# Kernel optimization log

Hardware: AMD Instinct MI355X
Metric: run time of the kernel (lower is better)

The kernel has to match this reference:

```python
import jax, jax.numpy as jnp
import numpy as np

D_MODEL = 1024
EPS = 1e-5  # torch LayerNorm default


def layernorm(x, gamma, beta):
    mu = jnp.mean(x, axis=-1, keepdims=True)
    var = jnp.mean(jnp.square(x - mu), axis=-1, keepdims=True)
    return (x - mu) * jax.lax.rsqrt(var + EPS) * gamma + beta


def setup_inputs() -> dict:
    key = jax.random.key(0)
    ks = jax.random.split(key, 9)
    B, S, D = 4, 2048, D_MODEL
    s = 1.0 / np.sqrt(D)  # ~ nn.Linear default init scale
    return {
        "x": jax.random.normal(ks[0], (B, S, D), dtype=jnp.float32),
        "wq_w": jax.random.uniform(ks[1], (D, D), jnp.float32, -s, s),
        "wq_b": jax.random.uniform(ks[2], (D,), jnp.float32, -s, s),
        "wk_w": jax.random.uniform(ks[3], (D, D), jnp.float32, -s, s),
        "wk_b": jax.random.uniform(ks[4], (D,), jnp.float32, -s, s),
        "wv_w": jax.random.uniform(ks[5], (D, D), jnp.float32, -s, s),
        "wv_b": jax.random.uniform(ks[6], (D,), jnp.float32, -s, s),
        "lin_w": jax.random.uniform(ks[7], (D, D), jnp.float32, -s, s),
        "lin_b": jax.random.uniform(ks[8], (D,), jnp.float32, -s, s),
        "g1": jnp.ones((D,), jnp.float32),
        "b1": jnp.zeros((D,), jnp.float32),
        "g2": jnp.ones((D,), jnp.float32),
        "b2": jnp.zeros((D,), jnp.float32),
    }


def reference(x, wq_w, wq_b, wk_w, wk_b, wv_w, wv_b, lin_w, lin_b, g1, b1, g2, b2):
    # single-head attention over full d_model (num_heads unused in original forward)
    q = jnp.einsum("bsd,ed->bse", x, wq_w) + wq_b
    k = jnp.einsum("bsd,ed->bse", x, wk_w) + wk_b
    v = jnp.einsum("bsd,ed->bse", x, wv_w) + wv_b
    scale = 1.0 / jnp.sqrt(jnp.float32(x.shape[-1]))
    scores = jax.nn.softmax(jnp.einsum("bqd,bkd->bqk", q, k) * scale, axis=2)
    attention = jnp.einsum("bqk,bkd->bqd", scores, v)
    # faithful to original: tril applied to the [S, D] attention OUTPUT per batch
    attention = jnp.tril(attention)
    x = layernorm(x + attention, g1, b1)
    linear_output = jnp.einsum("bsd,ed->bse", x, lin_w) + lin_b
    x = layernorm(x + linear_output, g2, b2)
    return x
```

## Files before the change

kernel.cpp:

```cpp
#include <hip/hip_runtime.h>
#include <hip/hip_bf16.h>

#define SEQ 2048
#define DM 1024
#define NB 4

typedef short bf16x8 __attribute__((ext_vector_type(8)));
typedef float f32x4 __attribute__((ext_vector_type(4)));
typedef float f32x4v __attribute__((ext_vector_type(4)));
typedef unsigned short u16x4 __attribute__((ext_vector_type(4)));
typedef unsigned short u16x8 __attribute__((ext_vector_type(8)));

__device__ __forceinline__ float bf2f(unsigned short u) {
  union { unsigned int i; float f; } w; w.i = ((unsigned int)u) << 16; return w.f;
}
__device__ __forceinline__ unsigned short f2bf(float f) {
  union { __hip_bfloat16 h; unsigned short u; } w; w.h = __float2bfloat16(f); return w.u;
}
__device__ __forceinline__ void load_lds16(const void* g, void* l) {
  __builtin_amdgcn_global_load_lds((const __attribute__((address_space(1))) void*)g,
                                   (__attribute__((address_space(3))) void*)l, 16, 0, 0);
}

__global__ __launch_bounds__(256) void cvt_kernel(const float* __restrict__ in,
                                                  unsigned short* __restrict__ out, int n4) {
  int idx = blockIdx.x * 256 + threadIdx.x;
  int stride = gridDim.x * 256;
  for (int i = idx; i < n4; i += stride) {
    f32x4v x = ((const f32x4v*)in)[i];
    u16x4 o;
    o[0] = f2bf(x[0]); o[1] = f2bf(x[1]); o[2] = f2bf(x[2]); o[3] = f2bf(x[3]);
    ((u16x4*)out)[i] = o;
  }
}

__global__ __launch_bounds__(256, 2) void gemm_bt(
    const unsigned short* __restrict__ A, int lda, long sA,
    const unsigned short* __restrict__ B, int ldb, long sB,
    void* __restrict__ Cv, int ldc, long sC,
    int K, const float* __restrict__ bias, float scale, int outf32)
{
  __shared__ unsigned short As[128 * 64];
  __shared__ unsigned short Bs[128 * 64];
  const int tid = threadIdx.x;
  const int lane = tid & 63;
  const int wave = tid >> 6;
  const int wm = wave >> 1, wn = wave & 1;
  const int m0 = blockIdx.x * 128, n0 = blockIdx.y * 128;
  const unsigned short* Ab = A + (size_t)sA * blockIdx.z;
  const unsigned short* Bb = B + (size_t)sB * blockIdx.z;

  f32x4 acc[4][4];
#pragma unroll
  for (int i = 0; i < 4; ++i)
#pragma unroll
    for (int j = 0; j < 4; ++j)
      acc[i][j] = (f32x4){0.f, 0.f, 0.f, 0.f};

  const int nk = K >> 6;
  for (int kt = 0; kt < nk; ++kt) {
    __syncthreads();
    const int kb = kt << 6;
#pragma unroll
    for (int it = 0; it < 4; ++it) {
      int c = it * 256 + tid;
      int row = c >> 3;
      int lslot = (c & 7) ^ (row & 7);
      int ldsoff = (it * 256 + wave * 64) * 8;
      load_lds16(Ab + (size_t)(m0 + row) * lda + kb + lslot * 8, &As[ldsoff]);
      load_lds16(Bb + (size_t)(n0 + row) * ldb + kb + lslot * 8, &Bs[ldsoff]);
    }
    __syncthreads();
#pragma unroll
    for (int h = 0; h < 2; ++h) {
      bf16x8 af[4], bfr[4];
#pragma unroll
      for (int i = 0; i < 4; ++i) {
        int row = wm * 64 + i * 16 + (lane & 15);
        int pslot = (h * 4 + (lane >> 4)) ^ (row & 7);
        af[i] = *(const bf16x8*)&As[row * 64 + pslot * 8];
      }
#pragma unroll
      for (int j = 0; j < 4; ++j) {
        int row = wn * 64 + j * 16 + (lane & 15);
        int pslot = (h * 4 + (lane >> 4)) ^ (row & 7);
        bfr[j] = *(const bf16x8*)&Bs[row * 64 + pslot * 8];
      }
#pragma unroll
      for (int i = 0; i < 4; ++i)
#pragma unroll
        for (int j = 0; j < 4; ++j)
          acc[i][j] = __builtin_amdgcn_mfma_f32_16x16x32_bf16(af[i], bfr[j], acc[i][j], 0, 0, 0);
    }
  }

  const int rsub = (lane >> 4) * 4;
  const int cbase = n0 + wn * 64 + (lane & 15);
  if (outf32) {
    float* C = (float*)Cv + (size_t)sC * blockIdx.z;
#pragma unroll
    for (int i = 0; i < 4; ++i) {
      int rbase = m0 + wm * 64 + i * 16 + rsub;
#pragma unroll
      for (int j = 0; j < 4; ++j)
#pragma unroll
        for (int r = 0; r < 4; ++r)
          C[(size_t)(rbase + r) * ldc + cbase + j * 16] = acc[i][j][r] * scale;
    }
  } else {
    unsigned short* C = (unsigned short*)Cv + (size_t)sC * blockIdx.z;
    float bv[4] = {0.f, 0.f, 0.f, 0.f};
    if (bias) {
#pragma unroll
      for (int j = 0; j < 4; ++j) bv[j] = bias[cbase + j * 16];
    }
#pragma unroll
    for (int i = 0; i < 4; ++i) {
      int rbase = m0 + wm * 64 + i * 16 + rsub;
#pragma unroll
      for (int j = 0; j < 4; ++j)
#pragma unroll
        for (int r = 0; r < 4; ++r)
          C[(size_t)(rbase + r) * ldc + cbase + j * 16] = f2bf(acc[i][j][r] + bv[j]);
    }
  }
}

__global__ __launch_bounds__(256) void transpose_kernel(const unsigned short* __restrict__ v,
                                                        int lda, long sV,
                                                        unsigned short* __restrict__ vt) {
  __shared__ unsigned short t[64][65];
  int b = blockIdx.z;
  int s0 = blockIdx.x * 64;
  int d0 = blockIdx.y * 64;
  int tid = threadIdx.x;
  int rr = tid >> 3;
  int c8 = (tid & 7) * 8;
  const unsigned short* vb = v + (size_t)sV * b;
#pragma unroll
  for (int it = 0; it < 2; ++it) {
    int row = rr + it * 32;
    u16x8 val = *(const u16x8*)&vb[(size_t)(s0 + row) * lda + d0 + c8];
#pragma unroll
    for (int j = 0; j < 8; ++j) t[row][c8 + j] = val[j];
  }
  __syncthreads();
#pragma unroll
  for (int it = 0; it < 2; ++it) {
    int drow = rr + it * 32;
    u16x8 o;
#pragma unroll
    for (int j = 0; j < 8; ++j) o[j] = t[c8 + j][drow];
    *(u16x8*)&vt[((size_t)b * DM + d0 + drow) * SEQ + s0 + c8] = o;
  }
}

__global__ __launch_bounds__(256) void softmax_kernel(const float* __restrict__ Sc,
                                                      unsigned short* __restrict__ P) {
  int row = blockIdx.x;
  int tid = threadIdx.x;
  const float* sr = Sc + (size_t)row * SEQ;
  float v[8];
  f32x4v a = ((const f32x4v*)sr)[tid * 2];
  f32x4v b = ((const f32x4v*)sr)[tid * 2 + 1];
  v[0]=a[0]; v[1]=a[1]; v[2]=a[2]; v[3]=a[3];
  v[4]=b[0]; v[5]=b[1]; v[6]=b[2]; v[7]=b[3];
  float m = v[0];
#pragma unroll
  for (int j = 1; j < 8; ++j) m = fmaxf(m, v[j]);
#pragma unroll
  for (int off = 32; off; off >>= 1) m = fmaxf(m, __shfl_xor(m, off));
  __shared__ float red[8];
  int wv = tid >> 6;
  if ((tid & 63) == 0) red[wv] = m;
  __syncthreads();
  m = fmaxf(fmaxf(red[0], red[1]), fmaxf(red[2], red[3]));
  float s = 0.f;
#pragma unroll
  for (int j = 0; j < 8; ++j) { v[j] = __expf(v[j] - m); s += v[j]; }
#pragma unroll
  for (int off = 32; off; off >>= 1) s += __shfl_xor(s, off);
  if ((tid & 63) == 0) red[4 + wv] = s;
  __syncthreads();
  s = red[4] + red[5] + red[6] + red[7];
  float inv = 1.f / s;
  u16x8 o;
#pragma unroll
  for (int j = 0; j < 8; ++j) o[j] = f2bf(v[j] * inv);
  *(u16x8*)&P[(size_t)row * SEQ + tid * 8] = o;
}

__global__ __launch_bounds__(256) void ln_kernel(
    const float* __restrict__ xf, const unsigned short* __restrict__ xb,
    const unsigned short* __restrict__ res, int masked,
    const float* __restrict__ g, const float* __restrict__ be,
    float* __restrict__ outf, unsigned short* __restrict__ outb)
{
  int row = blockIdx.x;
  int s = row & (SEQ - 1);
  int tid = threadIdx.x;
  int d0 = tid * 4;
  float v[4];
  if (xf) {
    f32x4v t = ((const f32x4v*)(xf + (size_t)row * DM))[tid];
    v[0]=t[0]; v[1]=t[1]; v[2]=t[2]; v[3]=t[3];
  } else {
    u16x4 t = ((const u16x4*)(xb + (size_t)row * DM))[tid];
    v[0]=bf2f(t[0]); v[1]=bf2f(t[1]); v[2]=bf2f(t[2]); v[3]=bf2f(t[3]);
  }
  u16x4 rv = ((const u16x4*)(res + (size_t)row * DM))[tid];
#pragma unroll
  for (int j = 0; j < 4; ++j) {
    float r = bf2f(rv[j]);
    if (masked && (d0 + j) > s) r = 0.f;
    v[j] += r;
  }
  float s1 = v[0] + v[1] + v[2] + v[3];
  float s2 = v[0]*v[0] + v[1]*v[1] + v[2]*v[2] + v[3]*v[3];
#pragma unroll
  for (int off = 32; off; off >>= 1) { s1 += __shfl_xor(s1, off); s2 += __shfl_xor(s2, off); }
  __shared__ float red[8];
  int wv = tid >> 6;
  if ((tid & 63) == 0) { red[wv] = s1; red[4 + wv] = s2; }
  __syncthreads();
  s1 = red[0] + red[1] + red[2] + red[3];
  s2 = red[4] + red[5] + red[6] + red[7];
  float mean = s1 * (1.f / DM);
  float var = s2 * (1.f / DM) - mean * mean;
  float rstd = rsqrtf(var + 1e-5f);
  f32x4v gv = ((const f32x4v*)g)[tid];
  f32x4v bv = ((const f32x4v*)be)[tid];
  if (outf) {
    f32x4v o;
#pragma unroll
    for (int j = 0; j < 4; ++j) o[j] = (v[j] - mean) * rstd * gv[j] + bv[j];
    ((f32x4v*)(outf + (size_t)row * DM))[tid] = o;
  } else {
    u16x4 o;
#pragma unroll
    for (int j = 0; j < 4; ++j) o[j] = f2bf((v[j] - mean) * rstd * gv[j] + bv[j]);
    ((u16x4*)(outb + (size_t)row * DM))[tid] = o;
  }
}

extern "C" void kernel_launch(void* const* d_in, const int* in_sizes, int n_in,
                              void* d_out, int out_size, void* d_ws, size_t ws_size,
                              hipStream_t stream) {
  (void)in_sizes; (void)n_in; (void)out_size; (void)ws_size;
  const float* x     = (const float*)d_in[0];
  const float* wq_w  = (const float*)d_in[1];
  const float* wq_b  = (const float*)d_in[2];
  const float* wk_w  = (const float*)d_in[3];
  const float* wk_b  = (const float*)d_in[4];
  const float* wv_w  = (const float*)d_in[5];
  const float* wv_b  = (const float*)d_in[6];
  const float* lin_w = (const float*)d_in[7];
  const float* lin_b = (const float*)d_in[8];
  const float* g1    = (const float*)d_in[9];
  const float* b1    = (const float*)d_in[10];
  const float* g2    = (const float*)d_in[11];
  const float* b2    = (const float*)d_in[12];

  const size_t MB = 1ull << 20;
  char* ws = (char*)d_ws;
  float*          sc   = (float*)(ws);
  unsigned short* attn = (unsigned short*)(ws);
  unsigned short* lin  = (unsigned short*)(ws + 16*MB);
  unsigned short* x1   = (unsigned short*)(ws + 32*MB);
  unsigned short* wqkvb= (unsigned short*)(ws + 48*MB);
  unsigned short* xb   = (unsigned short*)(ws + 54*MB);
  unsigned short* P    = (unsigned short*)(ws + 64*MB);
  unsigned short* qkv  = (unsigned short*)(ws + 96*MB);
  unsigned short* vt   = (unsigned short*)(ws + 144*MB);
  unsigned short* lwb  = (unsigned short*)(ws + 160*MB);
  float*          bqkv = (float*)(ws + 162*MB);

  const size_t SD = (size_t)NB * SEQ * DM;

  cvt_kernel<<<2048, 256, 0, stream>>>(x, xb, (int)(SD / 4));
  cvt_kernel<<<1024, 256, 0, stream>>>(wq_w, wqkvb, DM * DM / 4);
  cvt_kernel<<<1024, 256, 0, stream>>>(wk_w, wqkvb + DM * DM, DM * DM / 4);
  cvt_kernel<<<1024, 256, 0, stream>>>(wv_w, wqkvb + 2 * DM * DM, DM * DM / 4);
  cvt_kernel<<<1024, 256, 0, stream>>>(lin_w, lwb, DM * DM / 4);
  hipMemcpyAsync(bqkv,        wq_b, DM * sizeof(float), hipMemcpyDeviceToDevice, stream);
  hipMemcpyAsync(bqkv + DM,   wk_b, DM * sizeof(float), hipMemcpyDeviceToDevice, stream);
  hipMemcpyAsync(bqkv + 2*DM, wv_b, DM * sizeof(float), hipMemcpyDeviceToDevice, stream);

  gemm_bt<<<dim3(64, 24, 1), 256, 0, stream>>>(xb, DM, 0, wqkvb, DM, 0, qkv, 3 * DM, 0,
                                               DM, bqkv, 1.f, 0);
  transpose_kernel<<<dim3(SEQ / 64, DM / 64, NB), 256, 0, stream>>>(
      qkv + 2 * DM, 3 * DM, (long)SEQ * 3 * DM, vt);

  const float scale = 0.03125f;
  gemm_bt<<<dim3(16, 16, NB), 256, 0, stream>>>(
      qkv, 3 * DM, (long)SEQ * 3 * DM,
      qkv + DM, 3 * DM, (long)SEQ * 3 * DM,
      sc, SEQ, (long)SEQ * SEQ, DM, nullptr, scale, 1);
  softmax_kernel<<<NB * SEQ, 256, 0, stream>>>(sc, P);
  gemm_bt<<<dim3(16, 8, NB), 256, 0, stream>>>(
      P, SEQ, (long)SEQ * SEQ,
      vt, SEQ, (long)DM * SEQ,
      attn, DM, (long)SEQ * DM, SEQ, nullptr, 1.f, 0);

  ln_kernel<<<NB * SEQ, 256, 0, stream>>>(x, nullptr, attn, 1, g1, b1, nullptr, x1);
  gemm_bt<<<dim3(64, 8, 1), 256, 0, stream>>>(x1, DM, 0, lwb, DM, 0, lin, DM, 0, DM, lin_b, 1.f, 0);
  ln_kernel<<<NB * SEQ, 256, 0, stream>>>(nullptr, x1, lin, 0, g2, b2, (float*)d_out, nullptr);
}
```

Before: 235.7 us.

## Add 256-tile pipelined score GEMM, bf16 in-place scores, skip masked PV tiles

The QK^T scores GEMM moves to a new 256x256-tile, 512-thread kernel that double-buffers LDS loads and raises wave priority around the MFMA blocks. It writes scaled scores as bf16, and softmax then runs in place on that buffer, so the fp32 score matrix and the separate P buffer are no longer needed. The P·V GEMM gains a trilskip flag that exits early on output tiles lying entirely above the diagonal, since tril zeroes those attention outputs anyway. The trade-off is extra rounding of the pre-softmax scores to bf16. Skipped tiles also leave their attn entries unwritten, and this is only safe if the masked layernorm never reads those positions.

```diff
diff --git a/kernel.cpp b/kernel.cpp
--- a/kernel.cpp
+++ b/kernel.cpp
@@ -38,15 +38,16 @@
     const unsigned short* __restrict__ A, int lda, long sA,
     const unsigned short* __restrict__ B, int ldb, long sB,
     void* __restrict__ Cv, int ldc, long sC,
-    int K, const float* __restrict__ bias, float scale, int outf32)
+    int K, const float* __restrict__ bias, float scale, int outf32, int trilskip)
 {
+  const int m0 = blockIdx.x * 128, n0 = blockIdx.y * 128;
+  if (trilskip && n0 > m0 + 127) return;
   __shared__ unsigned short As[128 * 64];
   __shared__ unsigned short Bs[128 * 64];
   const int tid = threadIdx.x;
   const int lane = tid & 63;
   const int wave = tid >> 6;
   const int wm = wave >> 1, wn = wave & 1;
-  const int m0 = blockIdx.x * 128, n0 = blockIdx.y * 128;
   const unsigned short* Ab = A + (size_t)sA * blockIdx.z;
   const unsigned short* Bb = B + (size_t)sB * blockIdx.z;
 
@@ -121,7 +122,138 @@
       for (int j = 0; j < 4; ++j)
 #pragma unroll
         for (int r = 0; r < 4; ++r)
-          C[(size_t)(rbase + r) * ldc + cbase + j * 16] = f2bf(acc[i][j][r] + bv[j]);
+          C[(size_t)(rbase + r) * ldc + cbase + j * 16] = f2bf(acc[i][j][r] * scale + bv[j]);
+    }
+  }
+}
+
+__global__ __launch_bounds__(512, 2) void gemm256(
+    const unsigned short* __restrict__ A, int lda, long sA,
+    const unsigned short* __restrict__ B, int ldb, long sB,
+    void* __restrict__ Cv, int ldc, long sC,
+    int K, const float* __restrict__ bias, float scale, int outf32)
+{
+  __shared__ unsigned short As[2][256 * 64];
+  __shared__ unsigned short Bs[2][256 * 64];
+  const int tid = threadIdx.x;
+  const int lane = tid & 63;
+  const int wave = tid >> 6;
+  const int wm = wave >> 2;
+  const int wn = wave & 3;
+  const int m0 = blockIdx.x * 256, n0 = blockIdx.y * 256;
+  const unsigned short* Ab = A + (size_t)sA * blockIdx.z;
+  const unsigned short* Bb = B + (size_t)sB * blockIdx.z;
+
+  f32x4 acc[8][4];
+#pragma unroll
+  for (int i = 0; i < 8; ++i)
+#pragma unroll
+    for (int j = 0; j < 4; ++j)
+      acc[i][j] = (f32x4){0.f, 0.f, 0.f, 0.f};
+
+  const int nk = K >> 6;
+
+  auto STAGE = [&](int b, int kt) {
+    const int kb = kt << 6;
+#pragma unroll
+    for (int i = 0; i < 4; ++i) {
+      int c = i * 512 + tid;
+      int row = c >> 3;
+      int lslot = (c & 7) ^ (row & 7);
+      load_lds16(Ab + (size_t)(m0 + row) * lda + kb + lslot * 8, &As[b][c * 8]);
+      load_lds16(Bb + (size_t)(n0 + row) * ldb + kb + lslot * 8, &Bs[b][c * 8]);
+    }
+  };
+
+  STAGE(0, 0);
+  if (nk > 1) {
+    STAGE(1, 1);
+    asm volatile("s_waitcnt vmcnt(8)" ::: "memory");
+  } else {
+    asm volatile("s_waitcnt vmcnt(0)" ::: "memory");
+  }
+  __builtin_amdgcn_sched_barrier(0);
+  __builtin_amdgcn_s_barrier();
+  __builtin_amdgcn_sched_barrier(0);
+
+  for (int kt = 0; kt < nk; ++kt) {
+    const int b = kt & 1;
+    const unsigned short* Asb = As[b];
+    const unsigned short* Bsb = Bs[b];
+    bf16x8 bfr[4][2];
+#pragma unroll
+    for (int j = 0; j < 4; ++j) {
+      int row = wn * 64 + j * 16 + (lane & 15);
+#pragma unroll
+      for (int h = 0; h < 2; ++h) {
+        int pslot = (h * 4 + (lane >> 4)) ^ (row & 7);
+        bfr[j][h] = *(const bf16x8*)&Bsb[row * 64 + pslot * 8];
+      }
+    }
+#pragma unroll
+    for (int q = 0; q < 4; ++q) {
+      bf16x8 af[2][2];
+#pragma unroll
+      for (int i = 0; i < 2; ++i) {
+        int row = wm * 128 + (q * 2 + i) * 16 + (lane & 15);
+#pragma unroll
+        for (int h = 0; h < 2; ++h) {
+          int pslot = (h * 4 + (lane >> 4)) ^ (row & 7);
+          af[i][h] = *(const bf16x8*)&Asb[row * 64 + pslot * 8];
+        }
+      }
+      __builtin_amdgcn_s_setprio(1);
+#pragma unroll
+      for (int i = 0; i < 2; ++i)
+#pragma unroll
+        for (int j = 0; j < 4; ++j)
+#pragma unroll
+          for (int h = 0; h < 2; ++h)
+            acc[q * 2 + i][j] =
+                __builtin_amdgcn_mfma_f32_16x16x32_bf16(af[i][h], bfr[j][h], acc[q * 2 + i][j], 0, 0, 0);
+      __builtin_amdgcn_s_setprio(0);
+    }
+    __builtin_amdgcn_sched_barrier(0);
+    __builtin_amdgcn_s_barrier();
+    __builtin_amdgcn_sched_barrier(0);
+    if (kt + 2 < nk) STAGE(b, kt + 2);
+    if (kt + 1 < nk) {
+      if (kt + 2 < nk) asm volatile("s_waitcnt vmcnt(8)" ::: "memory");
+      else             asm volatile("s_waitcnt vmcnt(0)" ::: "memory");
+      __builtin_amdgcn_sched_barrier(0);
+      __builtin_amdgcn_s_barrier();
+      __builtin_amdgcn_sched_barrier(0);
+    }
+  }
+
+  const int rsub = (lane >> 4) * 4;
+  const int cbase = n0 + wn * 64 + (lane & 15);
+  if (outf32) {
+    float* C = (float*)Cv + (size_t)sC * blockIdx.z;
+#pragma unroll
+    for (int i = 0; i < 8; ++i) {
+      int rbase = m0 + wm * 128 + i * 16 + rsub;
+#pragma unroll
+      for (int j = 0; j < 4; ++j)
+#pragma unroll
+        for (int r = 0; r < 4; ++r)
+          C[(size_t)(rbase + r) * ldc + cbase + j * 16] = acc[i][j][r] * scale;
+    }
+  } else {
+    unsigned short* C = (unsigned short*)Cv + (size_t)sC * blockIdx.z;
+    float bv[4] = {0.f, 0.f, 0.f, 0.f};
+    if (bias) {
+#pragma unroll
+      for (int j = 0; j < 4; ++j) bv[j] = bias[cbase + j * 16];
+    }
+#pragma unroll
+    for (int i = 0; i < 8; ++i) {
+      int rbase = m0 + wm * 128 + i * 16 + rsub;
+#pragma unroll
+      for (int j = 0; j < 4; ++j)
+#pragma unroll
+        for (int r = 0; r < 4; ++r)
+          C[(size_t)(rbase + r) * ldc + cbase + j * 16] = f2bf(acc[i][j][r] * scale + bv[j]);
     }
   }
 }
@@ -155,16 +287,14 @@
   }
 }
 
-__global__ __launch_bounds__(256) void softmax_kernel(const float* __restrict__ Sc,
-                                                      unsigned short* __restrict__ P) {
+__global__ __launch_bounds__(256) void softmax_kernel(unsigned short* __restrict__ Sc) {
   int row = blockIdx.x;
   int tid = threadIdx.x;
-  const float* sr = Sc + (size_t)row * SEQ;
+  unsigned short* sr = Sc + (size_t)row * SEQ;
+  u16x8 raw = *(const u16x8*)&sr[tid * 8];
   float v[8];
-  f32x4v a = ((const f32x4v*)sr)[tid * 2];
-  f32x4v b = ((const f32x4v*)sr)[tid * 2 + 1];
-  v[0]=a[0]; v[1]=a[1]; v[2]=a[2]; v[3]=a[3];
-  v[4]=b[0]; v[5]=b[1]; v[6]=b[2]; v[7]=b[3];
+#pragma unroll
+  for (int j = 0; j < 8; ++j) v[j] = bf2f(raw[j]);
   float m = v[0];
 #pragma unroll
   for (int j = 1; j < 8; ++j) m = fmaxf(m, v[j]);
@@ -187,7 +317,7 @@
   u16x8 o;
 #pragma unroll
   for (int j = 0; j < 8; ++j) o[j] = f2bf(v[j] * inv);
-  *(u16x8*)&P[(size_t)row * SEQ + tid * 8] = o;
+  *(u16x8*)&sr[tid * 8] = o;
 }
 
 __global__ __launch_bounds__(256) void ln_kernel(
@@ -263,17 +393,16 @@
 
   const size_t MB = 1ull << 20;
   char* ws = (char*)d_ws;
-  float*          sc   = (float*)(ws);
-  unsigned short* attn = (unsigned short*)(ws);
-  unsigned short* lin  = (unsigned short*)(ws + 16*MB);
-  unsigned short* x1   = (unsigned short*)(ws + 32*MB);
-  unsigned short* wqkvb= (unsigned short*)(ws + 48*MB);
-  unsigned short* xb   = (unsigned short*)(ws + 54*MB);
-  unsigned short* P    = (unsigned short*)(ws + 64*MB);
-  unsigned short* qkv  = (unsigned short*)(ws + 96*MB);
-  unsigned short* vt   = (unsigned short*)(ws + 144*MB);
-  unsigned short* lwb  = (unsigned short*)(ws + 160*MB);
-  float*          bqkv = (float*)(ws + 162*MB);
+  unsigned short* scP  = (unsigned short*)(ws);
+  unsigned short* attn = (unsigned short*)(ws + 32*MB);
+  unsigned short* x1   = (unsigned short*)(ws + 48*MB);
+  unsigned short* lin  = (unsigned short*)(ws + 64*MB);
+  unsigned short* xb   = (unsigned short*)(ws + 80*MB);
+  unsigned short* wqkvb= (unsigned short*)(ws + 96*MB);
+  unsigned short* lwb  = (unsigned short*)(ws + 102*MB);
+  float*          bqkv = (float*)(ws + 104*MB);
+  unsigned short* qkv  = (unsigned short*)(ws + 112*MB);
+  unsigned short* vt   = (unsigned short*)(ws + 160*MB);
 
   const size_t SD = (size_t)NB * SEQ * DM;
 
@@ -287,22 +416,22 @@
   hipMemcpyAsync(bqkv + 2*DM, wv_b, DM * sizeof(float), hipMemcpyDeviceToDevice, stream);
 
   gemm_bt<<<dim3(64, 24, 1), 256, 0, stream>>>(xb, DM, 0, wqkvb, DM, 0, qkv, 3 * DM, 0,
-                                               DM, bqkv, 1.f, 0);
+                                               DM, bqkv, 1.f, 0, 0);
   transpose_kernel<<<dim3(SEQ / 64, DM / 64, NB), 256, 0, stream>>>(
       qkv + 2 * DM, 3 * DM, (long)SEQ * 3 * DM, vt);
 
   const float scale = 0.03125f;
-  gemm_bt<<<dim3(16, 16, NB), 256, 0, stream>>>(
+  gemm256<<<dim3(8, 8, NB), 512, 0, stream>>>(
       qkv, 3 * DM, (long)SEQ * 3 * DM,
       qkv + DM, 3 * DM, (long)SEQ * 3 * DM,
-      sc, SEQ, (long)SEQ * SEQ, DM, nullptr, scale, 1);
-  softmax_kernel<<<NB * SEQ, 256, 0, stream>>>(sc, P);
+      scP, SEQ, (long)SEQ * SEQ, DM, nullptr, scale, 0);
+  softmax_kernel<<<NB * SEQ, 256, 0, stream>>>(scP);
   gemm_bt<<<dim3(16, 8, NB), 256, 0, stream>>>(
-      P, SEQ, (long)SEQ * SEQ,
+      scP, SEQ, (long)SEQ * SEQ,
       vt, SEQ, (long)DM * SEQ,
-      attn, DM, (long)SEQ * DM, SEQ, nullptr, 1.f, 0);
+      attn, DM, (long)SEQ * DM, SEQ, nullptr, 1.f, 0, 1);
 
   ln_kernel<<<NB * SEQ, 256, 0, stream>>>(x, nullptr, attn, 1, g1, b1, nullptr, x1);
-  gemm_bt<<<dim3(64, 8, 1), 256, 0, stream>>>(x1, DM, 0, lwb, DM, 0, lin, DM, 0, DM, lin_b, 1.f, 0);
+  gemm_bt<<<dim3(64, 8, 1), 256, 0, stream>>>(x1, DM, 0, lwb, DM, 0, lin, DM, 0, DM, lin_b, 1.f, 0, 0);
   ln_kernel<<<NB * SEQ, 256, 0, stream>>>(nullptr, x1, lin, 0, g2, b2, (float*)d_out, nullptr);
 }
```

New measurement: 235.2 us. Within noise of the previous version (-0.2%).

## Fuse staging conversions, V transpose into QKV epilogue, bf16 scores, tril tile skip

Applied to the files above, without the earlier changes.

Merges the five conversion kernels and three bias memcpys into one staging kernel. Writes V transposed directly from the QKV GEMM epilogue, removing the separate transpose kernel. Stores attention scores as bf16 and runs softmax in place, which halves score traffic but lowers score precision before softmax. Skips the PV GEMM tiles that tril would zero, and LN1 now reads the bf16 copy of x instead of fp32, which adds rounding error.

```diff
diff --git a/kernel.cpp b/kernel.cpp
--- a/kernel.cpp
+++ b/kernel.cpp
@@ -21,16 +21,39 @@
   __builtin_amdgcn_global_load_lds((const __attribute__((address_space(1))) void*)g,
                                    (__attribute__((address_space(3))) void*)l, 16, 0, 0);
 }
-
-__global__ __launch_bounds__(256) void cvt_kernel(const float* __restrict__ in,
-                                                  unsigned short* __restrict__ out, int n4) {
+__device__ __forceinline__ void cvt4(const float* __restrict__ in,
+                                     unsigned short* __restrict__ out, int i) {
+  f32x4v v = ((const f32x4v*)in)[i];
+  u16x4 o;
+  o[0] = f2bf(v[0]); o[1] = f2bf(v[1]); o[2] = f2bf(v[2]); o[3] = f2bf(v[3]);
+  ((u16x4*)out)[i] = o;
+}
+
+__global__ __launch_bounds__(256) void stage_kernel(
+    const float* __restrict__ x,
+    const float* __restrict__ wq, const float* __restrict__ wk,
+    const float* __restrict__ wv, const float* __restrict__ lw,
+    const float* __restrict__ bq, const float* __restrict__ bk, const float* __restrict__ bv,
+    unsigned short* __restrict__ xb, unsigned short* __restrict__ wqkvb,
+    unsigned short* __restrict__ lwb, float* __restrict__ bqkv)
+{
+  const int XC = (NB * SEQ * DM) / 4;
+  const int WC = (DM * DM) / 4;
+  const int BC = (3 * DM) / 4;
+  const int total = XC + 4 * WC + BC;
   int idx = blockIdx.x * 256 + threadIdx.x;
   int stride = gridDim.x * 256;
-  for (int i = idx; i < n4; i += stride) {
-    f32x4v x = ((const f32x4v*)in)[i];
-    u16x4 o;
-    o[0] = f2bf(x[0]); o[1] = f2bf(x[1]); o[2] = f2bf(x[2]); o[3] = f2bf(x[3]);
-    ((u16x4*)out)[i] = o;
+  for (int i = idx; i < total; i += stride) {
+    if (i < XC) { cvt4(x, xb, i); continue; }
+    int j = i - XC;
+    if (j < WC)          { cvt4(wq, wqkvb, j); continue; }
+    if (j < 2 * WC)      { cvt4(wk, wqkvb + (size_t)DM * DM, j - WC); continue; }
+    if (j < 3 * WC)      { cvt4(wv, wqkvb + 2 * (size_t)DM * DM, j - 2 * WC); continue; }
+    if (j < 4 * WC)      { cvt4(lw, lwb, j - 3 * WC); continue; }
+    int c = j - 4 * WC;
+    const float* src = (c < 256) ? bq : ((c < 512) ? bk : bv);
+    int off = (c < 256) ? c : ((c < 512) ? c - 256 : c - 512);
+    ((f32x4v*)bqkv)[c] = ((const f32x4v*)src)[off];
   }
 }
 
@@ -38,15 +61,17 @@
     const unsigned short* __restrict__ A, int lda, long sA,
     const unsigned short* __restrict__ B, int ldb, long sB,
     void* __restrict__ Cv, int ldc, long sC,
-    int K, const float* __restrict__ bias, float scale, int outf32)
+    int K, const float* __restrict__ bias, float scale, int outf32, int trilskip,
+    unsigned short* __restrict__ vtOut, int vtBase)
 {
+  const int m0 = blockIdx.x * 128, n0 = blockIdx.y * 128;
+  if (trilskip && n0 > m0 + 127) return;
   __shared__ unsigned short As[128 * 64];
   __shared__ unsigned short Bs[128 * 64];
   const int tid = threadIdx.x;
   const int lane = tid & 63;
   const int wave = tid >> 6;
   const int wm = wave >> 1, wn = wave & 1;
-  const int m0 = blockIdx.x * 128, n0 = blockIdx.y * 128;
   const unsigned short* Ab = A + (size_t)sA * blockIdx.z;
   const unsigned short* Bb = B + (size_t)sB * blockIdx.z;
 
@@ -96,7 +121,27 @@
 
   const int rsub = (lane >> 4) * 4;
   const int cbase = n0 + wn * 64 + (lane & 15);
-  if (outf32) {
+  if (vtOut && n0 >= vtBase) {
+    float bv[4] = {0.f, 0.f, 0.f, 0.f};
+    if (bias) {
+#pragma unroll
+      for (int j = 0; j < 4; ++j) bv[j] = bias[cbase + j * 16];
+    }
+#pragma unroll
+    for (int i = 0; i < 4; ++i) {
+      int sg = m0 + wm * 64 + i * 16 + rsub;
+      int bb = sg >> 11;
+      int sl = sg & (SEQ - 1);
+#pragma unroll
+      for (int j = 0; j < 4; ++j) {
+        int d = cbase + j * 16 - vtBase;
+        u16x4 o;
+#pragma unroll
+        for (int r = 0; r < 4; ++r) o[r] = f2bf(acc[i][j][r] * scale + bv[j]);
+        *(u16x4*)&vtOut[((size_t)bb * DM + d) * SEQ + sl] = o;
+      }
+    }
+  } else if (outf32) {
     float* C = (float*)Cv + (size_t)sC * blockIdx.z;
 #pragma unroll
     for (int i = 0; i < 4; ++i) {
@@ -121,50 +166,19 @@
       for (int j = 0; j < 4; ++j)
 #pragma unroll
         for (int r = 0; r < 4; ++r)
-          C[(size_t)(rbase + r) * ldc + cbase + j * 16] = f2bf(acc[i][j][r] + bv[j]);
-    }
-  }
-}
-
-__global__ __launch_bounds__(256) void transpose_kernel(const unsigned short* __restrict__ v,
-                                                        int lda, long sV,
-                                                        unsigned short* __restrict__ vt) {
-  __shared__ unsigned short t[64][65];
-  int b = blockIdx.z;
-  int s0 = blockIdx.x * 64;
-  int d0 = blockIdx.y * 64;
-  int tid = threadIdx.x;
-  int rr = tid >> 3;
-  int c8 = (tid & 7) * 8;
-  const unsigned short* vb = v + (size_t)sV * b;
-#pragma unroll
-  for (int it = 0; it < 2; ++it) {
-    int row = rr + it * 32;
-    u16x8 val = *(const u16x8*)&vb[(size_t)(s0 + row) * lda + d0 + c8];
-#pragma unroll
-    for (int j = 0; j < 8; ++j) t[row][c8 + j] = val[j];
-  }
-  __syncthreads();
-#pragma unroll
-  for (int it = 0; it < 2; ++it) {
-    int drow = rr + it * 32;
-    u16x8 o;
-#pragma unroll
-    for (int j = 0; j < 8; ++j) o[j] = t[c8 + j][drow];
-    *(u16x8*)&vt[((size_t)b * DM + d0 + drow) * SEQ + s0 + c8] = o;
-  }
-}
-
-__global__ __launch_bounds__(256) void softmax_kernel(const float* __restrict__ Sc,
-                                                      unsigned short* __restrict__ P) {
+          C[(size_t)(rbase + r) * ldc + cbase + j * 16] = f2bf(acc[i][j][r] * scale + bv[j]);
+    }
+  }
+}
+
+__global__ __launch_bounds__(256) void softmax_kernel(unsigned short* __restrict__ Sc) {
   int row = blockIdx.x;
   int tid = threadIdx.x;
-  const float* sr = Sc + (size_t)row * SEQ;
+  unsigned short* sr = Sc + (size_t)row * SEQ;
+  u16x8 raw = *(const u16x8*)&sr[tid * 8];
   float v[8];
-  f32x4v a = ((const f32x4v*)sr)[tid * 2];
-  f32x4v b = ((const f32x4v*)sr)[tid * 2 + 1];
-  v[0]=a[0]; v[1]=a[1]; v[2]=a[2]; v[3]=a[3];
-  v[4]=b[0]; v[5]=b[1]; v[6]=b[2]; v[7]=b[3];
+#pragma unroll
+  for (int j = 0; j < 8; ++j) v[j] = bf2f(raw[j]);
   float m = v[0];
 #pragma unroll
   for (int j = 1; j < 8; ++j) m = fmaxf(m, v[j]);
@@ -187,7 +201,7 @@
   u16x8 o;
 #pragma unroll
   for (int j = 0; j < 8; ++j) o[j] = f2bf(v[j] * inv);
-  *(u16x8*)&P[(size_t)row * SEQ + tid * 8] = o;
+  *(u16x8*)&sr[tid * 8] = o;
 }
 
 __global__ __launch_bounds__(256) void ln_kernel(
@@ -263,46 +277,36 @@
 
   const size_t MB = 1ull << 20;
   char* ws = (char*)d_ws;
-  float*          sc   = (float*)(ws);
-  unsigned short* attn = (unsigned short*)(ws);
-  unsigned short* lin  = (unsigned short*)(ws + 16*MB);
-  unsigned short* x1   = (unsigned short*)(ws + 32*MB);
-  unsigned short* wqkvb= (unsigned short*)(ws + 48*MB);
-  unsigned short* xb   = (unsigned short*)(ws + 54*MB);
-  unsigned short* P    = (unsigned short*)(ws + 64*MB);
-  unsigned short* qkv  = (unsigned short*)(ws + 96*MB);
-  unsigned short* vt   = (unsigned short*)(ws + 144*MB);
-  unsigned short* lwb  = (unsigned short*)(ws + 160*MB);
-  float*          bqkv = (float*)(ws + 162*MB);
-
-  const size_t SD = (size_t)NB * SEQ * DM;
-
-  cvt_kernel<<<2048, 256, 0, stream>>>(x, xb, (int)(SD / 4));
-  cvt_kernel<<<1024, 256, 0, stream>>>(wq_w, wqkvb, DM * DM / 4);
-  cvt_kernel<<<1024, 256, 0, stream>>>(wk_w, wqkvb + DM * DM, DM * DM / 4);
-  cvt_kernel<<<1024, 256, 0, stream>>>(wv_w, wqkvb + 2 * DM * DM, DM * DM / 4);
-  cvt_kernel<<<1024, 256, 0, stream>>>(lin_w, lwb, DM * DM / 4);
-  hipMemcpyAsync(bqkv,        wq_b, DM * sizeof(float), hipMemcpyDeviceToDevice, stream);
-  hipMemcpyAsync(bqkv + DM,   wk_b, DM * sizeof(float), hipMemcpyDeviceToDevice, stream);
-  hipMemcpyAsync(bqkv + 2*DM, wv_b, DM * sizeof(float), hipMemcpyDeviceToDevice, stream);
+  unsigned short* scP  = (unsigned short*)(ws);
+  unsigned short* attn = (unsigned short*)(ws + 32*MB);
+  unsigned short* x1   = (unsigned short*)(ws + 48*MB);
+  unsigned short* lin  = (unsigned short*)(ws + 64*MB);
+  unsigned short* xb   = (unsigned short*)(ws + 80*MB);
+  unsigned short* wqkvb= (unsigned short*)(ws + 96*MB);
+  unsigned short* lwb  = (unsigned short*)(ws + 102*MB);
+  float*          bqkv = (float*)(ws + 104*MB);
+  unsigned short* qkv  = (unsigned short*)(ws + 112*MB);
+  unsigned short* vt   = (unsigned short*)(ws + 160*MB);
+
+  stage_kernel<<<2048, 256, 0, stream>>>(x, wq_w, wk_w, wv_w, lin_w, wq_b, wk_b, wv_b,
+                                         xb, wqkvb, lwb, bqkv);
 
   gemm_bt<<<dim3(64, 24, 1), 256, 0, stream>>>(xb, DM, 0, wqkvb, DM, 0, qkv, 3 * DM, 0,
-                                               DM, bqkv, 1.f, 0);
-  transpose_kernel<<<dim3(SEQ / 64, DM / 64, NB), 256, 0, stream>>>(
-      qkv + 2 * DM, 3 * DM, (long)SEQ * 3 * DM, vt);
+                                               DM, bqkv, 1.f, 0, 0, vt, 2 * DM);
 
   const float scale = 0.03125f;
   gemm_bt<<<dim3(16, 16, NB), 256, 0, stream>>>(
       qkv, 3 * DM, (long)SEQ * 3 * DM,
       qkv + DM, 3 * DM, (long)SEQ * 3 * DM,
-      sc, SEQ, (long)SEQ * SEQ, DM, nullptr, scale, 1);
-  softmax_kernel<<<NB * SEQ, 256, 0, stream>>>(sc, P);
+      scP, SEQ, (long)SEQ * SEQ, DM, nullptr, scale, 0, 0, nullptr, 0);
+  softmax_kernel<<<NB * SEQ, 256, 0, stream>>>(scP);
   gemm_bt<<<dim3(16, 8, NB), 256, 0, stream>>>(
-      P, SEQ, (long)SEQ * SEQ,
+      scP, SEQ, (long)SEQ * SEQ,
       vt, SEQ, (long)DM * SEQ,
-      attn, DM, (long)SEQ * DM, SEQ, nullptr, 1.f, 0);
-
-  ln_kernel<<<NB * SEQ, 256, 0, stream>>>(x, nullptr, attn, 1, g1, b1, nullptr, x1);
-  gemm_bt<<<dim3(64, 8, 1), 256, 0, stream>>>(x1, DM, 0, lwb, DM, 0, lin, DM, 0, DM, lin_b, 1.f, 0);
+      attn, DM, (long)SEQ * DM, SEQ, nullptr, 1.f, 0, 1, nullptr, 0);
+
+  ln_kernel<<<NB * SEQ, 256, 0, stream>>>(nullptr, xb, attn, 1, g1, b1, nullptr, x1);
+  gemm_bt<<<dim3(64, 8, 1), 256, 0, stream>>>(x1, DM, 0, lwb, DM, 0, lin, DM, 0, DM,
+                                              lin_b, 1.f, 0, 0, nullptr, 0);
   ln_kernel<<<NB * SEQ, 256, 0, stream>>>(nullptr, x1, lin, 0, g2, b2, (float*)d_out, nullptr);
 }
```

After: 209.0 us (median of 3 runs). -11.4%, faster.
